# Kernel optimization log

Measured on AMD Instinct MI355X. Metric: run time of the kernel, lower is better.

## Reference

```python
import jax, jax.numpy as jnp
import numpy as np

DIM = 1024
H = 16
DH = DIM // H
EPS = 1e-5
NEG = -1e38


def _layernorm(x, g, b):
    m = jnp.mean(x, axis=-1, keepdims=True)
    v = jnp.mean((x - m) ** 2, axis=-1, keepdims=True)
    return (x - m) / jnp.sqrt(v + EPS) * g + b


def setup_inputs() -> dict:
    key = jax.random.key(0)
    ks = jax.random.split(key, 12)
    B, Nq, Nk = 4, 1024, 1024
    Q = jax.random.normal(ks[0], (B, Nq, DIM), dtype=jnp.float32)
    K = jax.random.normal(ks[1], (B, Nk, DIM), dtype=jnp.float32)
    V = jax.random.normal(ks[2], (B, Nk, DIM), dtype=jnp.float32)
    mask_Q = jax.random.randint(ks[3], (B, Nq), 0, 2).astype(jnp.bool_)
    mask_K = jax.random.randint(ks[4], (B, Nk), 0, 2).astype(jnp.bool_)
    s = 0.02
    Wq = jax.random.normal(ks[5], (DIM, DIM), dtype=jnp.float32) * s
    Wk = jax.random.normal(ks[6], (DIM, DIM), dtype=jnp.float32) * s
    Wv = jax.random.normal(ks[7], (DIM, DIM), dtype=jnp.float32) * s
    Wo = jax.random.normal(ks[8], (DIM, DIM), dtype=jnp.float32) * s
    ln1_g = jnp.ones((DIM,), jnp.float32); ln1_b = jnp.zeros((DIM,), jnp.float32)
    ln2_g = jnp.ones((DIM,), jnp.float32); ln2_b = jnp.zeros((DIM,), jnp.float32)
    return {"Q": Q, "K": K, "V": V, "Wq": Wq, "Wk": Wk, "Wv": Wv, "Wo": Wo,
            "ln1_g": ln1_g, "ln1_b": ln1_b, "ln2_g": ln2_g, "ln2_b": ln2_b,
            "mask_Q": mask_Q, "mask_K": mask_K}


def reference(Q, K, V, Wq, Wk, Wv, Wo, ln1_g, ln1_b, ln2_g, ln2_b, mask_Q, mask_K):
    B, Nq, _ = Q.shape
    Nk = K.shape[1]
    # zero out padded tokens before projection (mask_tensors)
    Qm = jnp.where(mask_Q[..., None], 0.0, Q)
    Km = jnp.where(mask_K[..., None], 0.0, K)
    Vm = jnp.where(mask_K[..., None], 0.0, V)
    # projections (bias=False); torch Linear stores W as [out, in]
    Qp = Qm @ Wq.T
    Kp = Km @ Wk.T
    Vp = Vm @ Wv.T
    # split heads: [B, N, H, DH]
    Qh = Qp.reshape(B, Nq, H, DH)
    Kh = Kp.reshape(B, Nk, H, DH)
    Vh = Vp.reshape(B, Nk, H, DH)
    # NOTE: original scales by sqrt(dim_V), not sqrt(head_dim)
    scores = jnp.einsum('bqhd,bkhd->bhqk', Qh, Kh) / jnp.sqrt(jnp.float32(DIM))
    pad = mask_Q[:, None, :, None] | mask_K[:, None, None, :]  # [B,1,Nq,Nk]
    A = jax.nn.softmax(jnp.where(pad, NEG, scores), axis=-1)
    A = jnp.where(pad, 0.0, A)  # post-softmax masked_fill (dropout = identity in eval)
    O = jnp.einsum('bhqk,bkhd->bqhd', A, Vh).reshape(B, Nq, DIM)
    mq = mask_Q[..., None]
    # residual uses the PROJECTED Q
    O = Qp + O
    O = jnp.where(mq, 0.0, _layernorm(O, ln1_g, ln1_b))
    # masked fc_o then exact (non-tanh) GELU; gelu(0)=0 so masking commutes
    h = jnp.where(mq, 0.0, O @ Wo.T)
    O = O + jax.nn.gelu(h, approximate=False)
    O = jnp.where(mq, 0.0, _layernorm(O, ln2_g, ln2_b))
    return O
```

## Files before the change

### kernel.cpp

```cpp
#include <hip/hip_runtime.h>

#define NTOK 4096
#define AST 72

typedef _Float16 half4v __attribute__((ext_vector_type(4)));
typedef _Float16 half8 __attribute__((ext_vector_type(8)));
typedef float floatx4 __attribute__((ext_vector_type(4)));

__device__ __forceinline__ half8 cvt8(float4 a, float4 b) {
  half8 h;
  h[0] = (_Float16)a.x; h[1] = (_Float16)a.y; h[2] = (_Float16)a.z; h[3] = (_Float16)a.w;
  h[4] = (_Float16)b.x; h[5] = (_Float16)b.y; h[6] = (_Float16)b.z; h[7] = (_Float16)b.w;
  return h;
}

#if defined(__has_builtin)
#if __has_builtin(__builtin_amdgcn_global_load_lds)
#define HAS_GLL 1
#endif
#endif

#ifdef HAS_GLL
#define STAGE16(gp, lp)                                                        \
  __builtin_amdgcn_global_load_lds(                                           \
      (const __attribute__((address_space(1))) void*)(gp),                     \
      (__attribute__((address_space(3))) void*)(lp), 16, 0, 0)
#else
#define STAGE16(gp, lp)                                                        \
  do { *(half8*)((_Float16*)(lp) + lane * 8) = *(const half8*)(gp); } while (0)
#endif

__device__ __forceinline__ int mask_is_bytes(const int* p) {
  int bad = 0;
#pragma unroll
  for (int i = 0; i < 64; i++) bad |= (((unsigned int)p[i]) > 1u);
  return bad;
}

__global__ __launch_bounds__(256) void cvt_all(
    const float* __restrict__ Q, const float* __restrict__ K, const float* __restrict__ V,
    const float* __restrict__ Wq, const float* __restrict__ Wk, const float* __restrict__ Wv,
    const float* __restrict__ Wo,
    const int* __restrict__ srcQ, const int* __restrict__ srcK,
    _Float16* __restrict__ Xq, _Float16* __restrict__ Xk, _Float16* __restrict__ Xv,
    _Float16* __restrict__ Wqh, _Float16* __restrict__ Wkh, _Float16* __restrict__ Wvh,
    _Float16* __restrict__ Woh,
    int* __restrict__ dstQ, int* __restrict__ dstK)
{
  const int blk = blockIdx.x;
  if (blk >= 8192) {
    const int t = (blk - 8192) * 256 + threadIdx.x;
    const int bq = mask_is_bytes(srcQ);
    const int bk = mask_is_bytes(srcK);
    dstQ[t] = bq ? (int)((const unsigned char*)srcQ)[t] : srcQ[t];
    dstK[t] = bk ? (int)((const unsigned char*)srcK)[t] : srcK[t];
    return;
  }
  const float* src; _Float16* dst; size_t off;
  if      (blk < 2048) { src = Q;  dst = Xq;  off = (size_t)blk * 2048; }
  else if (blk < 4096) { src = K;  dst = Xk;  off = (size_t)(blk - 2048) * 2048; }
  else if (blk < 6144) { src = V;  dst = Xv;  off = (size_t)(blk - 4096) * 2048; }
  else if (blk < 6656) { src = Wq; dst = Wqh; off = (size_t)(blk - 6144) * 2048; }
  else if (blk < 7168) { src = Wk; dst = Wkh; off = (size_t)(blk - 6656) * 2048; }
  else if (blk < 7680) { src = Wv; dst = Wvh; off = (size_t)(blk - 7168) * 2048; }
  else                 { src = Wo; dst = Woh; off = (size_t)(blk - 7680) * 2048; }
  const size_t i = off + (size_t)threadIdx.x * 8;
  const float4 a = *(const float4*)(src + i);
  const float4 b = *(const float4*)(src + i + 4);
  *(half8*)(dst + i) = cvt8(a, b);
}

#define GEMM97_CORE(AH, BH)                                                    \
  __shared__ _Float16 sA[128 * 32];                                            \
  __shared__ _Float16 sB[128 * 32];                                            \
  const int t = threadIdx.x;                                                   \
  const int bn = blockIdx.x, bm = blockIdx.y;                                  \
  const int lane = t & 63, wv = t >> 6, quad = lane >> 4, l16 = lane & 15;     \
  const int wm = wv & 1, wn = wv >> 1;                                         \
  const int srow = wv * 32 + (lane >> 2);                                      \
  const int scol = (lane & 3) * 8;                                             \
  floatx4 acc[4][4] = {};                                                      \
  const _Float16* gA = AH + (size_t)(bm * 128 + srow) * 1024 + scol;           \
  const _Float16* gB = BH + (size_t)(bn * 128 + srow) * 1024 + scol;           \
  for (int kt = 0; kt < 32; kt++) {                                            \
    __syncthreads();                                                           \
    STAGE16(gA + kt * 32,         &sA[(wv * 32) * 32]);                        \
    STAGE16(gA + kt * 32 + 16384, &sA[(wv * 32 + 16) * 32]);                   \
    STAGE16(gB + kt * 32,         &sB[(wv * 32) * 32]);                        \
    STAGE16(gB + kt * 32 + 16384, &sB[(wv * 32 + 16) * 32]);                   \
    __syncthreads();                                                           \
    half8 af[4], bf[4];                                                        \
    _Pragma("unroll")                                                          \
    for (int s = 0; s < 4; s++)                                                \
      af[s] = *(const half8*)&sA[(wm * 64 + s * 16 + l16) * 32 + quad * 8];    \
    _Pragma("unroll")                                                          \
    for (int u = 0; u < 4; u++)                                                \
      bf[u] = *(const half8*)&sB[(wn * 64 + u * 16 + l16) * 32 + quad * 8];    \
    _Pragma("unroll")                                                          \
    for (int s = 0; s < 4; s++)                                                \
      _Pragma("unroll")                                                        \
      for (int u = 0; u < 4; u++)                                              \
        acc[s][u] = __builtin_amdgcn_mfma_f32_16x16x32_f16(af[s], bf[u],       \
                                                           acc[s][u], 0, 0, 0); \
  }

__global__ __launch_bounds__(256) void qkv_gemm(
    const _Float16* __restrict__ Xq, const _Float16* __restrict__ Xk,
    const _Float16* __restrict__ Xv,
    const _Float16* __restrict__ Wqh, const _Float16* __restrict__ Wkh,
    const _Float16* __restrict__ Wvh,
    const int* __restrict__ mQ, const int* __restrict__ mK,
    _Float16* __restrict__ Qh, _Float16* __restrict__ Kh, _Float16* __restrict__ Vh)
{
  const int z = blockIdx.z;
  const _Float16* AH = (z == 0) ? Xq : (z == 1) ? Xk : Xv;
  const _Float16* BH = (z == 0) ? Wqh : (z == 1) ? Wkh : Wvh;
  const int* msk = (z == 0) ? mQ : mK;
  _Float16* out = (z == 0) ? Qh : (z == 1) ? Kh : Vh;
  GEMM97_CORE(AH, BH)
#pragma unroll
  for (int s = 0; s < 4; s++)
#pragma unroll
    for (int rr = 0; rr < 4; rr++) {
      const int row = bm * 128 + wm * 64 + s * 16 + quad * 4 + rr;
      const int m = msk[row];
#pragma unroll
      for (int u = 0; u < 4; u++)
        out[(size_t)row * 1024 + bn * 128 + wn * 64 + u * 16 + l16] =
            m ? (_Float16)0.0f : (_Float16)acc[s][u][rr];
    }
}

__global__ __launch_bounds__(256) void gemm_wo(
    const _Float16* __restrict__ AH, const _Float16* __restrict__ BH,
    const float* __restrict__ X1, float* __restrict__ O2)
{
  __shared__ _Float16 sA[128 * 32];
  __shared__ _Float16 sB[64 * 32];
  const int t = threadIdx.x;
  const int bn = blockIdx.x, bm = blockIdx.y;
  const int lane = t & 63, wv = t >> 6, quad = lane >> 4, l16 = lane & 15;
  const int srowA = wv * 32 + (lane >> 2);
  const int srowB = wv * 16 + (lane >> 2);
  const int scol = (lane & 3) * 8;
  floatx4 acc[2][4] = {};
  const _Float16* gA = AH + (size_t)(bm * 128 + srowA) * 1024 + scol;
  const _Float16* gB = BH + (size_t)(bn * 64 + srowB) * 1024 + scol;
  for (int kt = 0; kt < 32; kt++) {
    __syncthreads();
    STAGE16(gA + kt * 32,         &sA[(wv * 32) * 32]);
    STAGE16(gA + kt * 32 + 16384, &sA[(wv * 32 + 16) * 32]);
    STAGE16(gB + kt * 32,         &sB[(wv * 16) * 32]);
    __syncthreads();
    half8 af[2], bf[4];
#pragma unroll
    for (int s = 0; s < 2; s++)
      af[s] = *(const half8*)&sA[(wv * 32 + s * 16 + l16) * 32 + quad * 8];
#pragma unroll
    for (int u = 0; u < 4; u++)
      bf[u] = *(const half8*)&sB[(u * 16 + l16) * 32 + quad * 8];
#pragma unroll
    for (int s = 0; s < 2; s++)
#pragma unroll
      for (int u = 0; u < 4; u++)
        acc[s][u] = __builtin_amdgcn_mfma_f32_16x16x32_f16(af[s], bf[u],
                                                           acc[s][u], 0, 0, 0);
  }
#pragma unroll
  for (int s = 0; s < 2; s++)
#pragma unroll
    for (int rr = 0; rr < 4; rr++) {
      const int row = bm * 128 + wv * 32 + s * 16 + quad * 4 + rr;
#pragma unroll
      for (int u = 0; u < 4; u++) {
        const size_t idx = (size_t)row * 1024 + bn * 64 + u * 16 + l16;
        const float hv = acc[s][u][rr];
        const float ge = 0.5f * hv * (1.0f + erff(hv * 0.70710678118654752f));
        O2[idx] = X1[idx] + ge;
      }
    }
}

__global__ __launch_bounds__(256) void v_transpose(
    const _Float16* __restrict__ Vh, _Float16* __restrict__ Vt)
{
  __shared__ _Float16 sT[64 * AST];
  const int t = threadIdx.x;
  const int kt = blockIdx.x, bh = blockIdx.y;
  const int b = bh >> 4, h = bh & 15;
  const int r = t >> 2, c0 = (t & 3) * 16;
  const _Float16* src = Vh + (size_t)(b * 1024 + kt * 64 + r) * 1024 + h * 64 + c0;
  *(half8*)&sT[r * AST + c0] = *(const half8*)src;
  *(half8*)&sT[r * AST + c0 + 8] = *(const half8*)(src + 8);
  __syncthreads();
  half8 o0, o1;
#pragma unroll
  for (int j = 0; j < 8; j++) o0[j] = sT[(c0 + j) * AST + r];
#pragma unroll
  for (int j = 0; j < 8; j++) o1[j] = sT[(c0 + 8 + j) * AST + r];
  _Float16* dst = Vt + ((size_t)bh * 64 + r) * 1024 + kt * 64 + c0;
  *(half8*)dst = o0;
  *(half8*)(dst + 8) = o1;
}

__global__ __launch_bounds__(256) void attn_mfma3(
    const _Float16* __restrict__ Qh, const _Float16* __restrict__ Kh,
    const _Float16* __restrict__ Vt, const int* __restrict__ maskQ,
    const int* __restrict__ maskK, float* __restrict__ O1)
{
  __shared__ _Float16 sK[64 * AST];
  __shared__ _Float16 sV[64 * AST];
  __shared__ _Float16 sQP[64 * AST];
  __shared__ float bias[1024];

  const int t = threadIdx.x;
  const int qt = blockIdx.x, bh = blockIdx.y;
  const int b = bh >> 4, h = bh & 15;
  const int q0 = qt * 64;
  const size_t base = (size_t)b * 1024;
  const int wv = t >> 6, lane = t & 63, quad = lane >> 4, l16 = lane & 15;
  const int r = t >> 2, c0 = (t & 3) * 16;

  const _Float16* kbase = Kh + (base + r) * 1024 + h * 64 + c0;
  const _Float16* vbase = Vt + ((size_t)bh * 64 + r) * 1024 + c0;
  half8 k0v = *(const half8*)kbase;
  half8 k1v = *(const half8*)(kbase + 8);
  half8 v0v = *(const half8*)vbase;
  half8 v1v = *(const half8*)(vbase + 8);

  for (int i = t; i < 1024; i += 256)
    bias[i] = maskK[b * 1024 + i] ? -1e30f : 0.0f;

  {
    const _Float16* qp = Qh + (base + q0 + r) * 1024 + h * 64 + c0;
    *(half8*)&sQP[r * AST + c0] = *(const half8*)qp;
    *(half8*)&sQP[r * AST + c0 + 8] = *(const half8*)(qp + 8);
  }
  __syncthreads();

  const half8 bq0 = *(const half8*)&sQP[(wv * 16 + l16) * AST + quad * 8];
  const half8 bq1 = *(const half8*)&sQP[(wv * 16 + l16) * AST + 32 + quad * 8];

  float l_i = 0.0f;
  floatx4 acc_o[4] = {};

  for (int kt = 0; kt < 16; kt++) {
    __syncthreads();
    *(half8*)&sK[r * AST + c0]     = k0v;
    *(half8*)&sK[r * AST + c0 + 8] = k1v;
    *(half8*)&sV[r * AST + c0]     = v0v;
    *(half8*)&sV[r * AST + c0 + 8] = v1v;
    __syncthreads();

    if (kt < 15) {
      const _Float16* kp = kbase + (size_t)(kt + 1) * 64 * 1024;
      const _Float16* vp = vbase + (kt + 1) * 64;
      k0v = *(const half8*)kp;
      k1v = *(const half8*)(kp + 8);
      v0v = *(const half8*)vp;
      v1v = *(const half8*)(vp + 8);
    }

    floatx4 s[4] = {};
    __builtin_amdgcn_s_setprio(1);
#pragma unroll
    for (int mt = 0; mt < 4; mt++) {
      const half8 ak0 = *(const half8*)&sK[(mt * 16 + l16) * AST + quad * 8];
      const half8 ak1 = *(const half8*)&sK[(mt * 16 + l16) * AST + 32 + quad * 8];
      s[mt] = __builtin_amdgcn_mfma_f32_16x16x32_f16(ak0, bq0, s[mt], 0, 0, 0);
      s[mt] = __builtin_amdgcn_mfma_f32_16x16x32_f16(ak1, bq1, s[mt], 0, 0, 0);
    }
    __builtin_amdgcn_s_setprio(0);

    float rsum = 0.0f;
#pragma unroll
    for (int mt = 0; mt < 4; mt++) {
      const float4 b4 = *(const float4*)&bias[kt * 64 + mt * 16 + quad * 4];
      const float p0 = __expf(s[mt][0] * 0.03125f + b4.x);
      const float p1 = __expf(s[mt][1] * 0.03125f + b4.y);
      const float p2 = __expf(s[mt][2] * 0.03125f + b4.z);
      const float p3 = __expf(s[mt][3] * 0.03125f + b4.w);
      s[mt][0] = p0; s[mt][1] = p1; s[mt][2] = p2; s[mt][3] = p3;
      rsum += (p0 + p1) + (p2 + p3);
    }
    rsum += __shfl_xor(rsum, 16);
    rsum += __shfl_xor(rsum, 32);
    l_i += rsum;

#pragma unroll
    for (int mt = 0; mt < 4; mt++) {
      half4v pv;
      pv[0] = (_Float16)s[mt][0]; pv[1] = (_Float16)s[mt][1];
      pv[2] = (_Float16)s[mt][2]; pv[3] = (_Float16)s[mt][3];
      *(half4v*)&sQP[(wv * 16 + l16) * AST + mt * 16 + quad * 4] = pv;
    }

    const half8 ap0 = *(const half8*)&sQP[(wv * 16 + l16) * AST + quad * 8];
    const half8 ap1 = *(const half8*)&sQP[(wv * 16 + l16) * AST + 32 + quad * 8];
    __builtin_amdgcn_s_setprio(1);
#pragma unroll
    for (int nt = 0; nt < 4; nt++) {
      const half8 bv0 = *(const half8*)&sV[(nt * 16 + l16) * AST + quad * 8];
      const half8 bv1 = *(const half8*)&sV[(nt * 16 + l16) * AST + 32 + quad * 8];
      acc_o[nt] = __builtin_amdgcn_mfma_f32_16x16x32_f16(ap0, bv0, acc_o[nt], 0, 0, 0);
      acc_o[nt] = __builtin_amdgcn_mfma_f32_16x16x32_f16(ap1, bv1, acc_o[nt], 0, 0, 0);
    }
    __builtin_amdgcn_s_setprio(0);
  }

  float il[4];
#pragma unroll
  for (int rr = 0; rr < 4; rr++) {
    const float lq = __shfl(l_i, quad * 4 + rr);
    il[rr] = (lq > 0.0f) ? 1.0f / lq : 0.0f;
  }
#pragma unroll
  for (int rr = 0; rr < 4; rr++) {
    const int row = q0 + wv * 16 + quad * 4 + rr;
    const int mq = maskQ[b * 1024 + row];
#pragma unroll
    for (int nt = 0; nt < 4; nt++) {
      const size_t gi = (base + row) * 1024 + h * 64 + nt * 16 + l16;
      O1[gi] = mq ? 0.0f : ((float)Qh[gi] + acc_o[nt][rr] * il[rr]);
    }
  }
}

__device__ __forceinline__ void ln_stats(float4 x, int t, float* mean, float* rinv) {
  float s = x.x + x.y + x.z + x.w;
  float s2 = x.x * x.x + x.y * x.y + x.z * x.z + x.w * x.w;
#pragma unroll
  for (int off = 32; off >= 1; off >>= 1) { s += __shfl_xor(s, off); s2 += __shfl_xor(s2, off); }
  __shared__ float red[8];
  __shared__ float sm[2];
  const int wv = t >> 6, lane = t & 63;
  if (lane == 0) { red[wv] = s; red[4 + wv] = s2; }
  __syncthreads();
  if (t == 0) {
    const float S = red[0] + red[1] + red[2] + red[3];
    const float S2 = red[4] + red[5] + red[6] + red[7];
    const float m = S * (1.0f / 1024.0f);
    const float v = S2 * (1.0f / 1024.0f) - m * m;
    sm[0] = m; sm[1] = rsqrtf(v + 1e-5f);
  }
  __syncthreads();
  *mean = sm[0]; *rinv = sm[1];
}

__global__ __launch_bounds__(256) void ln_f32(
    const float* __restrict__ X, const float* __restrict__ g,
    const float* __restrict__ bta, const int* __restrict__ mask,
    float* __restrict__ out)
{
  const int rr = blockIdx.x, t = threadIdx.x, c = 4 * t;
  const float4 x = *(const float4*)&X[(size_t)rr * 1024 + c];
  float mean, ri;
  ln_stats(x, t, &mean, &ri);
  const int msk = mask[rr];
  const float4 gg = *(const float4*)&g[c];
  const float4 bb = *(const float4*)&bta[c];
  float4 o;
  o.x = msk ? 0.f : (x.x - mean) * ri * gg.x + bb.x;
  o.y = msk ? 0.f : (x.y - mean) * ri * gg.y + bb.y;
  o.z = msk ? 0.f : (x.z - mean) * ri * gg.z + bb.z;
  o.w = msk ? 0.f : (x.w - mean) * ri * gg.w + bb.w;
  *(float4*)&out[(size_t)rr * 1024 + c] = o;
}

__global__ __launch_bounds__(256) void ln_f32h(
    const float* __restrict__ X, const float* __restrict__ g,
    const float* __restrict__ bta, const int* __restrict__ mask,
    float* __restrict__ out, _Float16* __restrict__ outh)
{
  const int rr = blockIdx.x, t = threadIdx.x, c = 4 * t;
  const float4 x = *(const float4*)&X[(size_t)rr * 1024 + c];
  float mean, ri;
  ln_stats(x, t, &mean, &ri);
  const int msk = mask[rr];
  const float4 gg = *(const float4*)&g[c];
  const float4 bb = *(const float4*)&bta[c];
  float4 o;
  o.x = msk ? 0.f : (x.x - mean) * ri * gg.x + bb.x;
  o.y = msk ? 0.f : (x.y - mean) * ri * gg.y + bb.y;
  o.z = msk ? 0.f : (x.z - mean) * ri * gg.z + bb.z;
  o.w = msk ? 0.f : (x.w - mean) * ri * gg.w + bb.w;
  const size_t idx = (size_t)rr * 1024 + c;
  *(float4*)&out[idx] = o;
  half4v hh;
  hh[0] = (_Float16)o.x; hh[1] = (_Float16)o.y;
  hh[2] = (_Float16)o.z; hh[3] = (_Float16)o.w;
  *(half4v*)&outh[idx] = hh;
}

extern "C" void kernel_launch(void* const* d_in, const int* in_sizes, int n_in,
                              void* d_out, int out_size, void* d_ws, size_t ws_size,
                              hipStream_t stream)
{
  const float* Q  = (const float*)d_in[0];
  const float* K  = (const float*)d_in[1];
  const float* V  = (const float*)d_in[2];
  const float* Wq = (const float*)d_in[3];
  const float* Wk = (const float*)d_in[4];
  const float* Wv = (const float*)d_in[5];
  const float* Wo = (const float*)d_in[6];
  const float* g1 = (const float*)d_in[7];
  const float* b1 = (const float*)d_in[8];
  const float* g2 = (const float*)d_in[9];
  const float* b2 = (const float*)d_in[10];
  float* out = (float*)d_out;

  char* base = (char*)d_ws;
  const size_t MB_ = 1024 * 1024;
  _Float16* Xq  = (_Float16*)(base +  0 * MB_);
  _Float16* Xk  = (_Float16*)(base +  8 * MB_);
  _Float16* Xv  = (_Float16*)(base + 16 * MB_);
  _Float16* Wqh = (_Float16*)(base + 24 * MB_);
  _Float16* Wkh = (_Float16*)(base + 26 * MB_);
  _Float16* Wvh = (_Float16*)(base + 28 * MB_);
  _Float16* Woh = (_Float16*)(base + 30 * MB_);
  _Float16* Qh  = (_Float16*)(base + 32 * MB_);
  _Float16* Kh  = (_Float16*)(base + 40 * MB_);
  _Float16* Vh  = (_Float16*)(base + 48 * MB_);
  _Float16* Vt  = (_Float16*)(base + 56 * MB_);
  float*    O1  = (float*)(base + 64 * MB_);
  int*      mQ  = (int*)(base + 80 * MB_);
  int*      mK  = mQ + NTOK;
  float*    X1  = (float*)(base + 0 * MB_);
  _Float16* X1h = (_Float16*)(base + 16 * MB_);
  float*    O2  = (float*)(base + 32 * MB_);

  const dim3 bb(256);
  cvt_all<<<dim3(8208), bb, 0, stream>>>(Q, K, V, Wq, Wk, Wv, Wo,
                                         (const int*)d_in[11], (const int*)d_in[12],
                                         Xq, Xk, Xv, Wqh, Wkh, Wvh, Woh, mQ, mK);
  qkv_gemm<<<dim3(8, 32, 3), bb, 0, stream>>>(Xq, Xk, Xv, Wqh, Wkh, Wvh,
                                              mQ, mK, Qh, Kh, Vh);
  v_transpose<<<dim3(16, 64), bb, 0, stream>>>(Vh, Vt);
  attn_mfma3<<<dim3(16, 64), bb, 0, stream>>>(Qh, Kh, Vt, mQ, mK, O1);
  ln_f32h<<<dim3(4096), bb, 0, stream>>>(O1, g1, b1, mQ, X1, X1h);
  gemm_wo<<<dim3(16, 32), bb, 0, stream>>>(X1h, Woh, X1, O2);
  ln_f32<<<dim3(4096), bb, 0, stream>>>(O2, g2, b2, mQ, out);
}
```

Before: 248.4 us.

## Swizzle attention LDS tiles, reorder grid rasterization, use exp2 in softmax

```diff
diff --git a/kernel.cpp b/kernel.cpp
--- a/kernel.cpp
+++ b/kernel.cpp
@@ -1,11 +1,12 @@
 #include <hip/hip_runtime.h>
 
 #define NTOK 4096
-#define AST 72
 
 typedef _Float16 half4v __attribute__((ext_vector_type(4)));
 typedef _Float16 half8 __attribute__((ext_vector_type(8)));
 typedef float floatx4 __attribute__((ext_vector_type(4)));
+
+#define SWZ(row, col) ((((row) * 64) + (col)) ^ (((row) & 7) << 3))
 
 __device__ __forceinline__ half8 cvt8(float4 a, float4 b) {
   half8 h;
@@ -74,7 +75,7 @@
   __shared__ _Float16 sA[128 * 32];                                            \
   __shared__ _Float16 sB[128 * 32];                                            \
   const int t = threadIdx.x;                                                   \
-  const int bn = blockIdx.x, bm = blockIdx.y;                                  \
+  const int bn = blockIdx.y, bm = blockIdx.x;                                  \
   const int lane = t & 63, wv = t >> 6, quad = lane >> 4, l16 = lane & 15;     \
   const int wm = wv & 1, wn = wv >> 1;                                         \
   const int srow = wv * 32 + (lane >> 2);                                      \
@@ -138,7 +139,7 @@
   __shared__ _Float16 sA[128 * 32];
   __shared__ _Float16 sB[64 * 32];
   const int t = threadIdx.x;
-  const int bn = blockIdx.x, bm = blockIdx.y;
+  const int bn = blockIdx.y, bm = blockIdx.x;
   const int lane = t & 63, wv = t >> 6, quad = lane >> 4, l16 = lane & 15;
   const int srowA = wv * 32 + (lane >> 2);
   const int srowB = wv * 16 + (lane >> 2);
@@ -181,23 +182,24 @@
     }
 }
 
+#define VTST 72
 __global__ __launch_bounds__(256) void v_transpose(
     const _Float16* __restrict__ Vh, _Float16* __restrict__ Vt)
 {
-  __shared__ _Float16 sT[64 * AST];
+  __shared__ _Float16 sT[64 * VTST];
   const int t = threadIdx.x;
   const int kt = blockIdx.x, bh = blockIdx.y;
   const int b = bh >> 4, h = bh & 15;
   const int r = t >> 2, c0 = (t & 3) * 16;
   const _Float16* src = Vh + (size_t)(b * 1024 + kt * 64 + r) * 1024 + h * 64 + c0;
-  *(half8*)&sT[r * AST + c0] = *(const half8*)src;
-  *(half8*)&sT[r * AST + c0 + 8] = *(const half8*)(src + 8);
+  *(half8*)&sT[r * VTST + c0] = *(const half8*)src;
+  *(half8*)&sT[r * VTST + c0 + 8] = *(const half8*)(src + 8);
   __syncthreads();
   half8 o0, o1;
 #pragma unroll
-  for (int j = 0; j < 8; j++) o0[j] = sT[(c0 + j) * AST + r];
-#pragma unroll
-  for (int j = 0; j < 8; j++) o1[j] = sT[(c0 + 8 + j) * AST + r];
+  for (int j = 0; j < 8; j++) o0[j] = sT[(c0 + j) * VTST + r];
+#pragma unroll
+  for (int j = 0; j < 8; j++) o1[j] = sT[(c0 + 8 + j) * VTST + r];
   _Float16* dst = Vt + ((size_t)bh * 64 + r) * 1024 + kt * 64 + c0;
   *(half8*)dst = o0;
   *(half8*)(dst + 8) = o1;
@@ -208,13 +210,13 @@
     const _Float16* __restrict__ Vt, const int* __restrict__ maskQ,
     const int* __restrict__ maskK, float* __restrict__ O1)
 {
-  __shared__ _Float16 sK[64 * AST];
-  __shared__ _Float16 sV[64 * AST];
-  __shared__ _Float16 sQP[64 * AST];
+  __shared__ _Float16 sK[64 * 64];
+  __shared__ _Float16 sV[64 * 64];
+  __shared__ _Float16 sQP[64 * 64];
   __shared__ float bias[1024];
 
   const int t = threadIdx.x;
-  const int qt = blockIdx.x, bh = blockIdx.y;
+  const int bh = blockIdx.x, qt = blockIdx.y;
   const int b = bh >> 4, h = bh & 15;
   const int q0 = qt * 64;
   const size_t base = (size_t)b * 1024;
@@ -233,23 +235,25 @@
 
   {
     const _Float16* qp = Qh + (base + q0 + r) * 1024 + h * 64 + c0;
-    *(half8*)&sQP[r * AST + c0] = *(const half8*)qp;
-    *(half8*)&sQP[r * AST + c0 + 8] = *(const half8*)(qp + 8);
+    *(half8*)&sQP[SWZ(r, c0)]     = *(const half8*)qp;
+    *(half8*)&sQP[SWZ(r, c0 + 8)] = *(const half8*)(qp + 8);
   }
   __syncthreads();
 
-  const half8 bq0 = *(const half8*)&sQP[(wv * 16 + l16) * AST + quad * 8];
-  const half8 bq1 = *(const half8*)&sQP[(wv * 16 + l16) * AST + 32 + quad * 8];
+  const half8 bq0 = *(const half8*)&sQP[SWZ(wv * 16 + l16, quad * 8)];
+  const half8 bq1 = *(const half8*)&sQP[SWZ(wv * 16 + l16, 32 + quad * 8)];
 
   float l_i = 0.0f;
   floatx4 acc_o[4] = {};
 
+  const float C2 = 0.0450842200277985f;
+
   for (int kt = 0; kt < 16; kt++) {
     __syncthreads();
-    *(half8*)&sK[r * AST + c0]     = k0v;
-    *(half8*)&sK[r * AST + c0 + 8] = k1v;
-    *(half8*)&sV[r * AST + c0]     = v0v;
-    *(half8*)&sV[r * AST + c0 + 8] = v1v;
+    *(half8*)&sK[SWZ(r, c0)]     = k0v;
+    *(half8*)&sK[SWZ(r, c0 + 8)] = k1v;
+    *(half8*)&sV[SWZ(r, c0)]     = v0v;
+    *(half8*)&sV[SWZ(r, c0 + 8)] = v1v;
     __syncthreads();
 
     if (kt < 15) {
@@ -265,8 +269,8 @@
     __builtin_amdgcn_s_setprio(1);
 #pragma unroll
     for (int mt = 0; mt < 4; mt++) {
-      const half8 ak0 = *(const half8*)&sK[(mt * 16 + l16) * AST + quad * 8];
-      const half8 ak1 = *(const half8*)&sK[(mt * 16 + l16) * AST + 32 + quad * 8];
+      const half8 ak0 = *(const half8*)&sK[SWZ(mt * 16 + l16, quad * 8)];
+      const half8 ak1 = *(const half8*)&sK[SWZ(mt * 16 + l16, 32 + quad * 8)];
       s[mt] = __builtin_amdgcn_mfma_f32_16x16x32_f16(ak0, bq0, s[mt], 0, 0, 0);
       s[mt] = __builtin_amdgcn_mfma_f32_16x16x32_f16(ak1, bq1, s[mt], 0, 0, 0);
     }
@@ -276,10 +280,10 @@
 #pragma unroll
     for (int mt = 0; mt < 4; mt++) {
       const float4 b4 = *(const float4*)&bias[kt * 64 + mt * 16 + quad * 4];
-      const float p0 = __expf(s[mt][0] * 0.03125f + b4.x);
-      const float p1 = __expf(s[mt][1] * 0.03125f + b4.y);
-      const float p2 = __expf(s[mt][2] * 0.03125f + b4.z);
-      const float p3 = __expf(s[mt][3] * 0.03125f + b4.w);
+      const float p0 = __builtin_amdgcn_exp2f(s[mt][0] * C2 + b4.x);
+      const float p1 = __builtin_amdgcn_exp2f(s[mt][1] * C2 + b4.y);
+      const float p2 = __builtin_amdgcn_exp2f(s[mt][2] * C2 + b4.z);
+      const float p3 = __builtin_amdgcn_exp2f(s[mt][3] * C2 + b4.w);
       s[mt][0] = p0; s[mt][1] = p1; s[mt][2] = p2; s[mt][3] = p3;
       rsum += (p0 + p1) + (p2 + p3);
     }
@@ -292,16 +296,16 @@
       half4v pv;
       pv[0] = (_Float16)s[mt][0]; pv[1] = (_Float16)s[mt][1];
       pv[2] = (_Float16)s[mt][2]; pv[3] = (_Float16)s[mt][3];
-      *(half4v*)&sQP[(wv * 16 + l16) * AST + mt * 16 + quad * 4] = pv;
-    }
-
-    const half8 ap0 = *(const half8*)&sQP[(wv * 16 + l16) * AST + quad * 8];
-    const half8 ap1 = *(const half8*)&sQP[(wv * 16 + l16) * AST + 32 + quad * 8];
+      *(half4v*)&sQP[SWZ(wv * 16 + l16, mt * 16 + quad * 4)] = pv;
+    }
+
+    const half8 ap0 = *(const half8*)&sQP[SWZ(wv * 16 + l16, quad * 8)];
+    const half8 ap1 = *(const half8*)&sQP[SWZ(wv * 16 + l16, 32 + quad * 8)];
     __builtin_amdgcn_s_setprio(1);
 #pragma unroll
     for (int nt = 0; nt < 4; nt++) {
-      const half8 bv0 = *(const half8*)&sV[(nt * 16 + l16) * AST + quad * 8];
-      const half8 bv1 = *(const half8*)&sV[(nt * 16 + l16) * AST + 32 + quad * 8];
+      const half8 bv0 = *(const half8*)&sV[SWZ(nt * 16 + l16, quad * 8)];
+      const half8 bv1 = *(const half8*)&sV[SWZ(nt * 16 + l16, 32 + quad * 8)];
       acc_o[nt] = __builtin_amdgcn_mfma_f32_16x16x32_f16(ap0, bv0, acc_o[nt], 0, 0, 0);
       acc_o[nt] = __builtin_amdgcn_mfma_f32_16x16x32_f16(ap1, bv1, acc_o[nt], 0, 0, 0);
     }
@@ -433,11 +437,11 @@
   cvt_all<<<dim3(8208), bb, 0, stream>>>(Q, K, V, Wq, Wk, Wv, Wo,
                                          (const int*)d_in[11], (const int*)d_in[12],
                                          Xq, Xk, Xv, Wqh, Wkh, Wvh, Woh, mQ, mK);
-  qkv_gemm<<<dim3(8, 32, 3), bb, 0, stream>>>(Xq, Xk, Xv, Wqh, Wkh, Wvh,
+  qkv_gemm<<<dim3(32, 8, 3), bb, 0, stream>>>(Xq, Xk, Xv, Wqh, Wkh, Wvh,
                                               mQ, mK, Qh, Kh, Vh);
   v_transpose<<<dim3(16, 64), bb, 0, stream>>>(Vh, Vt);
-  attn_mfma3<<<dim3(16, 64), bb, 0, stream>>>(Qh, Kh, Vt, mQ, mK, O1);
+  attn_mfma3<<<dim3(64, 16), bb, 0, stream>>>(Qh, Kh, Vt, mQ, mK, O1);
   ln_f32h<<<dim3(4096), bb, 0, stream>>>(O1, g1, b1, mQ, X1, X1h);
-  gemm_wo<<<dim3(16, 32), bb, 0, stream>>>(X1h, Woh, X1, O2);
+  gemm_wo<<<dim3(32, 16), bb, 0, stream>>>(X1h, Woh, X1, O2);
   ln_f32<<<dim3(4096), bb, 0, stream>>>(O2, g2, b2, mQ, out);
 }
```

Measured after the change: 252.8 us. About the same (+1.8%).
